# Optimization experiments

Measured on AMD Instinct MI355X. Metric: run time of the kernel, lower is better.

The kernel has to match this reference:

```python
import jax, jax.numpy as jnp
import numpy as np

T, D, I, E, K = 2048, 768, 2048, 8, 2


def setup_inputs() -> dict:
    key = jax.random.key(0)
    ks = jax.random.split(key, 9)
    x = jax.random.normal(ks[0], (T, D), jnp.float32)
    router_weight = jax.random.normal(ks[1], (E, D), jnp.float32) * 0.02
    shared_w_gate = jax.random.normal(ks[2], (I, D), jnp.float32) * 0.02
    shared_w_up = jax.random.normal(ks[3], (I, D), jnp.float32) * 0.02
    shared_w_down = jax.random.normal(ks[4], (D, I), jnp.float32) * 0.02
    # ternary quantized expert weights in {-1, 0, 1}
    expert_q_gate = jax.random.randint(ks[5], (E, I, D), 0, 3, jnp.int32) - 1
    expert_q_up = jax.random.randint(ks[6], (E, I, D), 0, 3, jnp.int32) - 1
    expert_q_down = jax.random.randint(ks[7], (E, D, I), 0, 3, jnp.int32) - 1
    # per-expert, per-matrix dequant scales (gate, up, down)
    expert_scales = jax.random.uniform(ks[8], (E, 3), jnp.float32) * 0.05 + 0.01
    return {
        "x": x,
        "router_weight": router_weight,
        "shared_w_gate": shared_w_gate,
        "shared_w_up": shared_w_up,
        "shared_w_down": shared_w_down,
        "expert_q_gate": expert_q_gate,
        "expert_q_up": expert_q_up,
        "expert_q_down": expert_q_down,
        "expert_scales": expert_scales,
        "top_k": K,
    }


def _swiglu(x, wg, wu, wd):
    # down( silu(gate(x)) * up(x) )
    return (jax.nn.silu(x @ wg.T) * (x @ wu.T)) @ wd.T


def reference(x, router_weight, shared_w_gate, shared_w_up, shared_w_down,
              expert_q_gate, expert_q_up, expert_q_down, expert_scales, top_k):
    # --- router: softmax -> top-k -> renormalize ---
    probs = jax.nn.softmax(x @ router_weight.T, axis=-1)            # [T, E]
    vals, idx = jax.lax.top_k(probs, top_k)                          # [T, K]
    vals = vals / jnp.sum(vals, axis=-1, keepdims=True)
    n_experts = router_weight.shape[0]
    # combine weights as dense [T, E] gate (one-hot scatter of top-k probs)
    gate = jnp.sum(jax.nn.one_hot(idx, n_experts, dtype=x.dtype) * vals[..., None], axis=1)

    # --- dequantize paged ternary experts: w = ternary * scale ---
    wg = expert_q_gate.astype(x.dtype) * expert_scales[:, 0, None, None]  # [E, I, D]
    wu = expert_q_up.astype(x.dtype) * expert_scales[:, 1, None, None]    # [E, I, D]
    wd = expert_q_down.astype(x.dtype) * expert_scales[:, 2, None, None]  # [E, D, I]

    # --- expert SwiGLU, computed per expert and combined with the gate ---
    h = jax.nn.silu(jnp.einsum('td,eid->tei', x, wg)) * jnp.einsum('td,eid->tei', x, wu)
    expert_out = jnp.einsum('tei,edi->ted', h, wd)                   # [T, E, D]
    moe_out = jnp.einsum('te,ted->td', gate, expert_out)             # [T, D]

    # --- always-on shared expert ---
    shared_out = _swiglu(x, shared_w_gate, shared_w_up, shared_w_down)
    return shared_out + moe_out
```

## Files before the change

### kernel.cpp

```cpp
#include <hip/hip_runtime.h>
#include <hip/hip_bf16.h>

#define TDIM 2048
#define DDIM 768
#define IDIM 2048
#define NEXP 8

typedef __bf16 v8bf __attribute__((ext_vector_type(8)));
typedef float v4f __attribute__((ext_vector_type(4)));

#define MFMA_B16(A,B,C) __builtin_amdgcn_mfma_f32_16x16x32_bf16(A,B,C,0,0,0)

typedef __attribute__((address_space(1))) const unsigned int* gas_t;
typedef __attribute__((address_space(3))) unsigned int* las_t;

__device__ __forceinline__ void gload16(const void* g, void* l) {
  __builtin_amdgcn_global_load_lds((gas_t)g, (las_t)l, 16, 0, 0);
}

__global__ __launch_bounds__(64)
void router_kernel(const float* __restrict__ x, const float* __restrict__ rw,
                   int* __restrict__ cnt, int* __restrict__ lists, float* __restrict__ wt)
{
  const int t = blockIdx.x;
  const int lane = threadIdx.x;
  const float* xp = x + (size_t)t * DDIM;
  float4 xv0 = *(const float4*)(xp + lane * 4);
  float4 xv1 = *(const float4*)(xp + 256 + lane * 4);
  float4 xv2 = *(const float4*)(xp + 512 + lane * 4);
  float logit[NEXP];
#pragma unroll
  for (int e = 0; e < NEXP; ++e) {
    const float* w = rw + (size_t)e * DDIM;
    float4 w0 = *(const float4*)(w + lane * 4);
    float4 w1 = *(const float4*)(w + 256 + lane * 4);
    float4 w2 = *(const float4*)(w + 512 + lane * 4);
    float p = xv0.x * w0.x + xv0.y * w0.y + xv0.z * w0.z + xv0.w * w0.w
            + xv1.x * w1.x + xv1.y * w1.y + xv1.z * w1.z + xv1.w * w1.w
            + xv2.x * w2.x + xv2.y * w2.y + xv2.z * w2.z + xv2.w * w2.w;
#pragma unroll
    for (int off = 32; off > 0; off >>= 1) p += __shfl_down(p, off, 64);
    logit[e] = p;
  }
  if (lane == 0) {
    float m = logit[0];
#pragma unroll
    for (int e = 1; e < NEXP; ++e) m = fmaxf(m, logit[e]);
    float pr[NEXP];
#pragma unroll
    for (int e = 0; e < NEXP; ++e) pr[e] = expf(logit[e] - m);
    int i0 = 0; float v0 = pr[0];
#pragma unroll
    for (int e = 1; e < NEXP; ++e) if (pr[e] > v0) { v0 = pr[e]; i0 = e; }
    int i1 = -1; float v1 = -1.f;
#pragma unroll
    for (int e = 0; e < NEXP; ++e) if (e != i0 && pr[e] > v1) { v1 = pr[e]; i1 = e; }
    float inv = 1.f / (v0 + v1);
    int p0 = atomicAdd(&cnt[i0], 1);
    lists[i0 * TDIM + p0] = t * 2;
    wt[t * 2] = v0 * inv;
    int p1 = atomicAdd(&cnt[i1], 1);
    lists[i1 * TDIM + p1] = t * 2 + 1;
    wt[t * 2 + 1] = v1 * inv;
  }
}

template<bool ISINT>
__global__ __launch_bounds__(256)
void pack_tiles_kernel(const void* __restrict__ srcv, __hip_bfloat16* __restrict__ dst,
                       int NT, int KT)
{
  const int b = blockIdx.x;
  const int kt = b % KT;
  const int nt = (b / KT) % NT;
  const int e  = b / (KT * NT);
  const int N  = NT * 128;
  const int Kk = KT * 64;
  const int tid = threadIdx.x;
  __hip_bfloat16* dbase = dst + (size_t)b * 8192;
#pragma unroll
  for (int p = 0; p < 4; ++p) {
    const int q = p * 256 + tid;
    const int row = q >> 3;
    const int cb = ((q & 7) * 16) ^ ((row & 7) << 4);
    const int k = kt * 64 + (cb >> 1);
    const size_t srcoff = ((size_t)e * N + (nt * 128 + row)) * Kk + k;
    v8bf v;
    if constexpr (ISINT) {
      const int* s = (const int*)srcv + srcoff;
      int4 a0 = *(const int4*)s;
      int4 a1 = *(const int4*)(s + 4);
      v[0] = (__bf16)(float)a0.x; v[1] = (__bf16)(float)a0.y;
      v[2] = (__bf16)(float)a0.z; v[3] = (__bf16)(float)a0.w;
      v[4] = (__bf16)(float)a1.x; v[5] = (__bf16)(float)a1.y;
      v[6] = (__bf16)(float)a1.z; v[7] = (__bf16)(float)a1.w;
    } else {
      const float* s = (const float*)srcv + srcoff;
      float4 a0 = *(const float4*)s;
      float4 a1 = *(const float4*)(s + 4);
      v[0] = (__bf16)a0.x; v[1] = (__bf16)a0.y; v[2] = (__bf16)a0.z; v[3] = (__bf16)a0.w;
      v[4] = (__bf16)a1.x; v[5] = (__bf16)a1.y; v[6] = (__bf16)a1.z; v[7] = (__bf16)a1.w;
    }
    *(v8bf*)(dbase + (size_t)q * 8) = v;
  }
}

__global__ __launch_bounds__(256)
void pack_x_kernel(const float* __restrict__ src, __hip_bfloat16* __restrict__ dst)
{
  const size_t i = ((size_t)blockIdx.x * 256 + threadIdx.x) * 8;
  float4 a0 = *(const float4*)(src + i);
  float4 a1 = *(const float4*)(src + i + 4);
  v8bf v;
  v[0] = (__bf16)a0.x; v[1] = (__bf16)a0.y; v[2] = (__bf16)a0.z; v[3] = (__bf16)a0.w;
  v[4] = (__bf16)a1.x; v[5] = (__bf16)a1.y; v[6] = (__bf16)a1.z; v[7] = (__bf16)a1.w;
  *(v8bf*)(dst + i) = v;
}

__global__ __launch_bounds__(256)
void gateup_kernel(const __hip_bfloat16* __restrict__ xb,
                   const __hip_bfloat16* __restrict__ wgT, const __hip_bfloat16* __restrict__ wuT,
                   const __hip_bfloat16* __restrict__ sgT, const __hip_bfloat16* __restrict__ suT,
                   const float* __restrict__ es,
                   const int* __restrict__ cnt, const int* __restrict__ lists,
                   __hip_bfloat16* __restrict__ he, __hip_bfloat16* __restrict__ hs)
{
  const int b = blockIdx.x;
  int tm, tn, count;
  const __hip_bfloat16 *wg, *wu;
  const int* listE = nullptr;
  __hip_bfloat16* hout;
  float sg, su;
  if (b < 2048) {
    const int e = b >> 8; tm = (b >> 4) & 15; tn = b & 15;
    count = cnt[e];
    if (tm * 128 >= count) return;
    wg = wgT + (size_t)(e * 16 + tn) * (12 * 8192);
    wu = wuT + (size_t)(e * 16 + tn) * (12 * 8192);
    listE = lists + e * TDIM;
    sg = es[e * 3 + 0]; su = es[e * 3 + 1];
    hout = he;
  } else {
    const int b2 = b - 2048; tm = b2 >> 4; tn = b2 & 15;
    count = TDIM;
    wg = sgT + (size_t)tn * (12 * 8192);
    wu = suT + (size_t)tn * (12 * 8192);
    sg = 1.f; su = 1.f;
    hout = hs;
  }

  __shared__ __align__(16) char As[16384];
  __shared__ __align__(16) char Bg[16384];
  __shared__ __align__(16) char Bu[16384];

  const int tid = threadIdx.x;
  const int lane = tid & 63;
  const int wid = tid >> 6;
  const int wr = wid >> 1, wc = wid & 1;
  const int lr16 = lane & 15, hk = lane >> 4;
  const int xorm = (lr16 & 7) << 4;

  const int cA = (((lane & 7) ^ (lane >> 3)) << 4);
  const char* aptr[4];
#pragma unroll
  for (int p = 0; p < 4; ++p) {
    const int row = p * 32 + wid * 8 + (lane >> 3);
    const int rg = tm * 128 + row;
    int tok;
    if (listE) { const int idx = rg < count ? rg : count - 1; tok = listE[idx] >> 1; }
    else tok = rg;
    aptr[p] = (const char*)xb + (size_t)tok * (DDIM * 2) + cA;
  }
  const char* bgp = (const char*)wg + wid * 1024 + lane * 16;
  const char* bup = (const char*)wu + wid * 1024 + lane * 16;
  char* ldsA  = As + wid * 1024;
  char* ldsBg = Bg + wid * 1024;
  char* ldsBu = Bu + wid * 1024;

  v4f ag[4][4] = {};
  v4f au[4][4] = {};

  for (int kt = 0; kt < 12; ++kt) {
#pragma unroll
    for (int p = 0; p < 4; ++p) gload16(aptr[p] + kt * 128, ldsA + p * 4096);
#pragma unroll
    for (int p = 0; p < 4; ++p) gload16(bgp + kt * 16384 + p * 4096, ldsBg + p * 4096);
#pragma unroll
    for (int p = 0; p < 4; ++p) gload16(bup + kt * 16384 + p * 4096, ldsBu + p * 4096);
    __syncthreads();
#pragma unroll
    for (int ks = 0; ks < 2; ++ks) {
      const int colb = (ks * 64 + hk * 16) ^ xorm;
      v8bf fa[4];
#pragma unroll
      for (int m = 0; m < 4; ++m)
        fa[m] = *(const v8bf*)(As + (wr * 64 + m * 16 + lr16) * 128 + colb);
#pragma unroll
      for (int n = 0; n < 4; ++n) {
        v8bf fg = *(const v8bf*)(Bg + (wc * 64 + n * 16 + lr16) * 128 + colb);
        v8bf fu = *(const v8bf*)(Bu + (wc * 64 + n * 16 + lr16) * 128 + colb);
#pragma unroll
        for (int m = 0; m < 4; ++m) {
          ag[m][n] = MFMA_B16(fa[m], fg, ag[m][n]);
          au[m][n] = MFMA_B16(fa[m], fu, au[m][n]);
        }
      }
    }
    __syncthreads();
  }

#pragma unroll
  for (int m = 0; m < 4; ++m) {
#pragma unroll
    for (int j = 0; j < 4; ++j) {
      const int rl = wr * 64 + m * 16 + hk * 4 + j;
      const int rg = tm * 128 + rl;
      if (rg >= count) continue;
      const size_t drow = listE ? (size_t)listE[rg] : (size_t)rg;
      __hip_bfloat16* dst = hout + drow * IDIM + tn * 128 + wc * 64 + lr16;
#pragma unroll
      for (int n = 0; n < 4; ++n) {
        const float g = ag[m][n][j] * sg;
        const float u = au[m][n][j] * su;
        const float h = g / (1.f + __expf(-g)) * u;
        dst[n * 16] = __float2bfloat16(h);
      }
    }
  }
}

__global__ __launch_bounds__(256)
void down_kernel(const __hip_bfloat16* __restrict__ he, const __hip_bfloat16* __restrict__ hs,
                 const __hip_bfloat16* __restrict__ wdT, const __hip_bfloat16* __restrict__ sdT,
                 const float* __restrict__ es, const float* __restrict__ wt,
                 const int* __restrict__ cnt, const int* __restrict__ lists,
                 float* __restrict__ out)
{
  const int b = blockIdx.x;
  int tm, tn, count;
  const __hip_bfloat16 *wd, *asrc;
  const int* listE = nullptr;
  float sd;
  if (b < 768) {
    const int e = b / 96; const int r = b % 96; tm = r / 6; tn = r % 6;
    count = cnt[e];
    if (tm * 128 >= count) return;
    wd = wdT + (size_t)(e * 6 + tn) * (32 * 8192);
    listE = lists + e * TDIM;
    sd = es[e * 3 + 2];
    asrc = he;
  } else {
    const int r = b - 768; tm = r / 6; tn = r % 6;
    count = TDIM;
    wd = sdT + (size_t)tn * (32 * 8192);
    sd = 1.f;
    asrc = hs;
  }

  __shared__ __align__(16) char As[16384];
  __shared__ __align__(16) char Bs[16384];

  const int tid = threadIdx.x;
  const int lane = tid & 63;
  const int wid = tid >> 6;
  const int wr = wid >> 1, wc = wid & 1;
  const int lr16 = lane & 15, hk = lane >> 4;
  const int xorm = (lr16 & 7) << 4;

  const int cA = (((lane & 7) ^ (lane >> 3)) << 4);
  const char* aptr[4];
#pragma unroll
  for (int p = 0; p < 4; ++p) {
    const int row = p * 32 + wid * 8 + (lane >> 3);
    const int rg = tm * 128 + row;
    int srow;
    if (listE) { const int idx = rg < count ? rg : count - 1; srow = listE[idx]; }
    else srow = rg;
    aptr[p] = (const char*)asrc + (size_t)srow * (IDIM * 2) + cA;
  }
  const char* bp = (const char*)wd + wid * 1024 + lane * 16;
  char* ldsA = As + wid * 1024;
  char* ldsB = Bs + wid * 1024;

  v4f acc[4][4] = {};

  for (int kt = 0; kt < 32; ++kt) {
#pragma unroll
    for (int p = 0; p < 4; ++p) gload16(aptr[p] + kt * 128, ldsA + p * 4096);
#pragma unroll
    for (int p = 0; p < 4; ++p) gload16(bp + kt * 16384 + p * 4096, ldsB + p * 4096);
    __syncthreads();
#pragma unroll
    for (int ks = 0; ks < 2; ++ks) {
      const int colb = (ks * 64 + hk * 16) ^ xorm;
      v8bf fa[4];
#pragma unroll
      for (int m = 0; m < 4; ++m)
        fa[m] = *(const v8bf*)(As + (wr * 64 + m * 16 + lr16) * 128 + colb);
#pragma unroll
      for (int n = 0; n < 4; ++n) {
        v8bf fb = *(const v8bf*)(Bs + (wc * 64 + n * 16 + lr16) * 128 + colb);
#pragma unroll
        for (int m = 0; m < 4; ++m) acc[m][n] = MFMA_B16(fa[m], fb, acc[m][n]);
      }
    }
    __syncthreads();
  }

#pragma unroll
  for (int m = 0; m < 4; ++m) {
#pragma unroll
    for (int j = 0; j < 4; ++j) {
      const int rl = wr * 64 + m * 16 + hk * 4 + j;
      const int rg = tm * 128 + rl;
      if (rg >= count) continue;
      int tok; float w;
      if (listE) { const int slot = listE[rg]; tok = slot >> 1; w = wt[slot] * sd; }
      else { tok = rg; w = 1.f; }
      float* dst = out + (size_t)tok * DDIM + tn * 128 + wc * 64 + lr16;
#pragma unroll
      for (int n = 0; n < 4; ++n) atomicAdd(dst + n * 16, acc[m][n][j] * w);
    }
  }
}

extern "C" void kernel_launch(void* const* d_in, const int* in_sizes, int n_in,
                              void* d_out, int out_size, void* d_ws, size_t ws_size,
                              hipStream_t stream)
{
  const float* x   = (const float*)d_in[0];
  const float* rw  = (const float*)d_in[1];
  const float* swg = (const float*)d_in[2];
  const float* swu = (const float*)d_in[3];
  const float* swd = (const float*)d_in[4];
  const int*   qg  = (const int*)d_in[5];
  const int*   qu  = (const int*)d_in[6];
  const int*   qd  = (const int*)d_in[7];
  const float* es  = (const float*)d_in[8];
  float* out = (float*)d_out;

  char* ws = (char*)d_ws;
  size_t off = 0;
  auto alloc = [&](size_t bytes) { void* p = ws + off; off = (off + bytes + 255) & ~(size_t)255; return p; };
  int*   cnt   = (int*)alloc(NEXP * 4);
  int*   lists = (int*)alloc((size_t)NEXP * TDIM * 4);
  float* wt    = (float*)alloc((size_t)2 * TDIM * 4);
  __hip_bfloat16* xb  = (__hip_bfloat16*)alloc((size_t)TDIM * DDIM * 2);
  __hip_bfloat16* wgT = (__hip_bfloat16*)alloc((size_t)NEXP * 16 * 12 * 8192 * 2);
  __hip_bfloat16* wuT = (__hip_bfloat16*)alloc((size_t)NEXP * 16 * 12 * 8192 * 2);
  __hip_bfloat16* wdT = (__hip_bfloat16*)alloc((size_t)NEXP * 6 * 32 * 8192 * 2);
  __hip_bfloat16* sgT = (__hip_bfloat16*)alloc((size_t)16 * 12 * 8192 * 2);
  __hip_bfloat16* suT = (__hip_bfloat16*)alloc((size_t)16 * 12 * 8192 * 2);
  __hip_bfloat16* sdT = (__hip_bfloat16*)alloc((size_t)6 * 32 * 8192 * 2);
  __hip_bfloat16* hs  = (__hip_bfloat16*)alloc((size_t)TDIM * IDIM * 2);
  __hip_bfloat16* he  = (__hip_bfloat16*)alloc((size_t)2 * TDIM * IDIM * 2);

  hipMemsetAsync(cnt, 0, NEXP * 4, stream);
  hipMemsetAsync(out, 0, (size_t)TDIM * DDIM * 4, stream);

  router_kernel<<<TDIM, 64, 0, stream>>>(x, rw, cnt, lists, wt);
  pack_x_kernel<<<(TDIM * DDIM) / 2048, 256, 0, stream>>>(x, xb);
  pack_tiles_kernel<true><<<NEXP * 16 * 12, 256, 0, stream>>>(qg, wgT, 16, 12);
  pack_tiles_kernel<true><<<NEXP * 16 * 12, 256, 0, stream>>>(qu, wuT, 16, 12);
  pack_tiles_kernel<true><<<NEXP * 6 * 32, 256, 0, stream>>>(qd, wdT, 6, 32);
  pack_tiles_kernel<false><<<16 * 12, 256, 0, stream>>>(swg, sgT, 16, 12);
  pack_tiles_kernel<false><<<16 * 12, 256, 0, stream>>>(swu, suT, 16, 12);
  pack_tiles_kernel<false><<<6 * 32, 256, 0, stream>>>(swd, sdT, 6, 32);

  gateup_kernel<<<2048 + 256, 256, 0, stream>>>(xb, wgT, wuT, sgT, suT, es, cnt, lists, he, hs);
  down_kernel<<<768 + 96, 256, 0, stream>>>(he, hs, wdT, sdT, es, wt, cnt, lists, out);
}
```

Baseline: 422.9 us.

## Fuse pack kernels into one launch and halve GEMM N-tiles for more blocks

Merges the six weight-packing launches and the x-to-bf16 conversion into a single kernel that dispatches on block index, which removes per-launch overhead and lets the small conversions run alongside each other. The gate/up and down GEMM kernels now use 128x64 output tiles instead of 128x128 by addressing half of each packed 128-row weight tile, doubling the block count. Smaller LDS and accumulator footprints plus occupancy hints in launch_bounds are meant to keep more blocks resident and balance the uneven per-expert work. The cost is that each A tile is loaded from global memory twice as often and there are more atomic-add blocks in the down projection.

```diff
diff --git a/kernel.cpp b/kernel.cpp
--- a/kernel.cpp
+++ b/kernel.cpp
@@ -65,19 +65,41 @@
   }
 }
 
-template<bool ISINT>
 __global__ __launch_bounds__(256)
-void pack_tiles_kernel(const void* __restrict__ srcv, __hip_bfloat16* __restrict__ dst,
-                       int NT, int KT)
+void pack_all_kernel(const int* __restrict__ qg, const int* __restrict__ qu,
+                     const int* __restrict__ qd,
+                     const float* __restrict__ sg, const float* __restrict__ su,
+                     const float* __restrict__ sd, const float* __restrict__ x,
+                     __hip_bfloat16* __restrict__ wgT, __hip_bfloat16* __restrict__ wuT,
+                     __hip_bfloat16* __restrict__ wdT, __hip_bfloat16* __restrict__ sgT,
+                     __hip_bfloat16* __restrict__ suT, __hip_bfloat16* __restrict__ sdT,
+                     __hip_bfloat16* __restrict__ xb)
 {
   const int b = blockIdx.x;
-  const int kt = b % KT;
-  const int nt = (b / KT) % NT;
-  const int e  = b / (KT * NT);
+  const int tid = threadIdx.x;
+  if (b >= 5184) {
+    const size_t i = (size_t)(b - 5184) * 2048 + tid * 8;
+    float4 a0 = *(const float4*)(x + i);
+    float4 a1 = *(const float4*)(x + i + 4);
+    v8bf v;
+    v[0] = (__bf16)a0.x; v[1] = (__bf16)a0.y; v[2] = (__bf16)a0.z; v[3] = (__bf16)a0.w;
+    v[4] = (__bf16)a1.x; v[5] = (__bf16)a1.y; v[6] = (__bf16)a1.z; v[7] = (__bf16)a1.w;
+    *(v8bf*)(xb + i) = v;
+    return;
+  }
+  const void* src; __hip_bfloat16* dst; int NT, KT, isint, tile;
+  if (b < 1536)      { src = qg; dst = wgT; NT = 16; KT = 12; isint = 1; tile = b; }
+  else if (b < 3072) { src = qu; dst = wuT; NT = 16; KT = 12; isint = 1; tile = b - 1536; }
+  else if (b < 4608) { src = qd; dst = wdT; NT = 6;  KT = 32; isint = 1; tile = b - 3072; }
+  else if (b < 4800) { src = sg; dst = sgT; NT = 16; KT = 12; isint = 0; tile = b - 4608; }
+  else if (b < 4992) { src = su; dst = suT; NT = 16; KT = 12; isint = 0; tile = b - 4800; }
+  else               { src = sd; dst = sdT; NT = 6;  KT = 32; isint = 0; tile = b - 4992; }
+  const int kt = tile % KT;
+  const int nt = (tile / KT) % NT;
+  const int e  = tile / (KT * NT);
   const int N  = NT * 128;
   const int Kk = KT * 64;
-  const int tid = threadIdx.x;
-  __hip_bfloat16* dbase = dst + (size_t)b * 8192;
+  __hip_bfloat16* dbase = dst + (size_t)tile * 8192;
 #pragma unroll
   for (int p = 0; p < 4; ++p) {
     const int q = p * 256 + tid;
@@ -86,8 +108,8 @@
     const int k = kt * 64 + (cb >> 1);
     const size_t srcoff = ((size_t)e * N + (nt * 128 + row)) * Kk + k;
     v8bf v;
-    if constexpr (ISINT) {
-      const int* s = (const int*)srcv + srcoff;
+    if (isint) {
+      const int* s = (const int*)src + srcoff;
       int4 a0 = *(const int4*)s;
       int4 a1 = *(const int4*)(s + 4);
       v[0] = (__bf16)(float)a0.x; v[1] = (__bf16)(float)a0.y;
@@ -95,7 +117,7 @@
       v[4] = (__bf16)(float)a1.x; v[5] = (__bf16)(float)a1.y;
       v[6] = (__bf16)(float)a1.z; v[7] = (__bf16)(float)a1.w;
     } else {
-      const float* s = (const float*)srcv + srcoff;
+      const float* s = (const float*)src + srcoff;
       float4 a0 = *(const float4*)s;
       float4 a1 = *(const float4*)(s + 4);
       v[0] = (__bf16)a0.x; v[1] = (__bf16)a0.y; v[2] = (__bf16)a0.z; v[3] = (__bf16)a0.w;
@@ -105,19 +127,7 @@
   }
 }
 
-__global__ __launch_bounds__(256)
-void pack_x_kernel(const float* __restrict__ src, __hip_bfloat16* __restrict__ dst)
-{
-  const size_t i = ((size_t)blockIdx.x * 256 + threadIdx.x) * 8;
-  float4 a0 = *(const float4*)(src + i);
-  float4 a1 = *(const float4*)(src + i + 4);
-  v8bf v;
-  v[0] = (__bf16)a0.x; v[1] = (__bf16)a0.y; v[2] = (__bf16)a0.z; v[3] = (__bf16)a0.w;
-  v[4] = (__bf16)a1.x; v[5] = (__bf16)a1.y; v[6] = (__bf16)a1.z; v[7] = (__bf16)a1.w;
-  *(v8bf*)(dst + i) = v;
-}
-
-__global__ __launch_bounds__(256)
+__global__ __launch_bounds__(256, 3)
 void gateup_kernel(const __hip_bfloat16* __restrict__ xb,
                    const __hip_bfloat16* __restrict__ wgT, const __hip_bfloat16* __restrict__ wuT,
                    const __hip_bfloat16* __restrict__ sgT, const __hip_bfloat16* __restrict__ suT,
@@ -127,38 +137,39 @@
 {
   const int b = blockIdx.x;
   int tm, tn, count;
-  const __hip_bfloat16 *wg, *wu;
+  const char *wg, *wu;
   const int* listE = nullptr;
   __hip_bfloat16* hout;
   float sg, su;
-  if (b < 2048) {
-    const int e = b >> 8; tm = (b >> 4) & 15; tn = b & 15;
+  if (b < 4096) {
+    const int e = b >> 9; tm = (b >> 5) & 15; tn = b & 31;
     count = cnt[e];
     if (tm * 128 >= count) return;
-    wg = wgT + (size_t)(e * 16 + tn) * (12 * 8192);
-    wu = wuT + (size_t)(e * 16 + tn) * (12 * 8192);
+    const size_t base = (size_t)(e * 16 + (tn >> 1)) * (12 * 16384) + (tn & 1) * 8192;
+    wg = (const char*)wgT + base;
+    wu = (const char*)wuT + base;
     listE = lists + e * TDIM;
     sg = es[e * 3 + 0]; su = es[e * 3 + 1];
     hout = he;
   } else {
-    const int b2 = b - 2048; tm = b2 >> 4; tn = b2 & 15;
+    const int b2 = b - 4096; tm = b2 >> 5; tn = b2 & 31;
     count = TDIM;
-    wg = sgT + (size_t)tn * (12 * 8192);
-    wu = suT + (size_t)tn * (12 * 8192);
+    const size_t base = (size_t)(tn >> 1) * (12 * 16384) + (tn & 1) * 8192;
+    wg = (const char*)sgT + base;
+    wu = (const char*)suT + base;
     sg = 1.f; su = 1.f;
     hout = hs;
   }
 
   __shared__ __align__(16) char As[16384];
-  __shared__ __align__(16) char Bg[16384];
-  __shared__ __align__(16) char Bu[16384];
+  __shared__ __align__(16) char Bg[8192];
+  __shared__ __align__(16) char Bu[8192];
 
   const int tid = threadIdx.x;
   const int lane = tid & 63;
   const int wid = tid >> 6;
   const int wr = wid >> 1, wc = wid & 1;
   const int lr16 = lane & 15, hk = lane >> 4;
-  const int xorm = (lr16 & 7) << 4;
 
   const int cA = (((lane & 7) ^ (lane >> 3)) << 4);
   const char* aptr[4];
@@ -171,34 +182,38 @@
     else tok = rg;
     aptr[p] = (const char*)xb + (size_t)tok * (DDIM * 2) + cA;
   }
-  const char* bgp = (const char*)wg + wid * 1024 + lane * 16;
-  const char* bup = (const char*)wu + wid * 1024 + lane * 16;
+  const char* bgp = wg + wid * 1024 + lane * 16;
+  const char* bup = wu + wid * 1024 + lane * 16;
   char* ldsA  = As + wid * 1024;
   char* ldsBg = Bg + wid * 1024;
   char* ldsBu = Bu + wid * 1024;
 
-  v4f ag[4][4] = {};
-  v4f au[4][4] = {};
+  v4f ag[4][2] = {};
+  v4f au[4][2] = {};
 
   for (int kt = 0; kt < 12; ++kt) {
 #pragma unroll
     for (int p = 0; p < 4; ++p) gload16(aptr[p] + kt * 128, ldsA + p * 4096);
 #pragma unroll
-    for (int p = 0; p < 4; ++p) gload16(bgp + kt * 16384 + p * 4096, ldsBg + p * 4096);
-#pragma unroll
-    for (int p = 0; p < 4; ++p) gload16(bup + kt * 16384 + p * 4096, ldsBu + p * 4096);
+    for (int p = 0; p < 2; ++p) gload16(bgp + kt * 16384 + p * 4096, ldsBg + p * 4096);
+#pragma unroll
+    for (int p = 0; p < 2; ++p) gload16(bup + kt * 16384 + p * 4096, ldsBu + p * 4096);
     __syncthreads();
 #pragma unroll
     for (int ks = 0; ks < 2; ++ks) {
-      const int colb = (ks * 64 + hk * 16) ^ xorm;
+      const int colb = ks * 64 + hk * 16;
       v8bf fa[4];
 #pragma unroll
-      for (int m = 0; m < 4; ++m)
-        fa[m] = *(const v8bf*)(As + (wr * 64 + m * 16 + lr16) * 128 + colb);
-#pragma unroll
-      for (int n = 0; n < 4; ++n) {
-        v8bf fg = *(const v8bf*)(Bg + (wc * 64 + n * 16 + lr16) * 128 + colb);
-        v8bf fu = *(const v8bf*)(Bu + (wc * 64 + n * 16 + lr16) * 128 + colb);
+      for (int m = 0; m < 4; ++m) {
+        const int r = wr * 64 + m * 16 + lr16;
+        fa[m] = *(const v8bf*)(As + r * 128 + (colb ^ ((r & 7) << 4)));
+      }
+#pragma unroll
+      for (int n = 0; n < 2; ++n) {
+        const int r = wc * 32 + n * 16 + lr16;
+        const int sb = r * 128 + (colb ^ ((r & 7) << 4));
+        v8bf fg = *(const v8bf*)(Bg + sb);
+        v8bf fu = *(const v8bf*)(Bu + sb);
 #pragma unroll
         for (int m = 0; m < 4; ++m) {
           ag[m][n] = MFMA_B16(fa[m], fg, ag[m][n]);
@@ -217,9 +232,9 @@
       const int rg = tm * 128 + rl;
       if (rg >= count) continue;
       const size_t drow = listE ? (size_t)listE[rg] : (size_t)rg;
-      __hip_bfloat16* dst = hout + drow * IDIM + tn * 128 + wc * 64 + lr16;
-#pragma unroll
-      for (int n = 0; n < 4; ++n) {
+      __hip_bfloat16* dst = hout + drow * IDIM + tn * 64 + wc * 32 + lr16;
+#pragma unroll
+      for (int n = 0; n < 2; ++n) {
         const float g = ag[m][n][j] * sg;
         const float u = au[m][n][j] * su;
         const float h = g / (1.f + __expf(-g)) * u;
@@ -229,7 +244,7 @@
   }
 }
 
-__global__ __launch_bounds__(256)
+__global__ __launch_bounds__(256, 4)
 void down_kernel(const __hip_bfloat16* __restrict__ he, const __hip_bfloat16* __restrict__ hs,
                  const __hip_bfloat16* __restrict__ wdT, const __hip_bfloat16* __restrict__ sdT,
                  const float* __restrict__ es, const float* __restrict__ wt,
@@ -238,34 +253,34 @@
 {
   const int b = blockIdx.x;
   int tm, tn, count;
-  const __hip_bfloat16 *wd, *asrc;
+  const char* wd;
+  const __hip_bfloat16* asrc;
   const int* listE = nullptr;
   float sd;
-  if (b < 768) {
-    const int e = b / 96; const int r = b % 96; tm = r / 6; tn = r % 6;
+  if (b < 1536) {
+    const int e = b / 192; const int r = b % 192; tm = r / 12; tn = r % 12;
     count = cnt[e];
     if (tm * 128 >= count) return;
-    wd = wdT + (size_t)(e * 6 + tn) * (32 * 8192);
+    wd = (const char*)wdT + (size_t)(e * 6 + (tn >> 1)) * (32 * 16384) + (tn & 1) * 8192;
     listE = lists + e * TDIM;
     sd = es[e * 3 + 2];
     asrc = he;
   } else {
-    const int r = b - 768; tm = r / 6; tn = r % 6;
+    const int r = b - 1536; tm = r / 12; tn = r % 12;
     count = TDIM;
-    wd = sdT + (size_t)tn * (32 * 8192);
+    wd = (const char*)sdT + (size_t)(tn >> 1) * (32 * 16384) + (tn & 1) * 8192;
     sd = 1.f;
     asrc = hs;
   }
 
   __shared__ __align__(16) char As[16384];
-  __shared__ __align__(16) char Bs[16384];
+  __shared__ __align__(16) char Bs[8192];
 
   const int tid = threadIdx.x;
   const int lane = tid & 63;
   const int wid = tid >> 6;
   const int wr = wid >> 1, wc = wid & 1;
   const int lr16 = lane & 15, hk = lane >> 4;
-  const int xorm = (lr16 & 7) << 4;
 
   const int cA = (((lane & 7) ^ (lane >> 3)) << 4);
   const char* aptr[4];
@@ -278,28 +293,31 @@
     else srow = rg;
     aptr[p] = (const char*)asrc + (size_t)srow * (IDIM * 2) + cA;
   }
-  const char* bp = (const char*)wd + wid * 1024 + lane * 16;
+  const char* bp = wd + wid * 1024 + lane * 16;
   char* ldsA = As + wid * 1024;
   char* ldsB = Bs + wid * 1024;
 
-  v4f acc[4][4] = {};
+  v4f acc[4][2] = {};
 
   for (int kt = 0; kt < 32; ++kt) {
 #pragma unroll
     for (int p = 0; p < 4; ++p) gload16(aptr[p] + kt * 128, ldsA + p * 4096);
 #pragma unroll
-    for (int p = 0; p < 4; ++p) gload16(bp + kt * 16384 + p * 4096, ldsB + p * 4096);
+    for (int p = 0; p < 2; ++p) gload16(bp + kt * 16384 + p * 4096, ldsB + p * 4096);
     __syncthreads();
 #pragma unroll
     for (int ks = 0; ks < 2; ++ks) {
-      const int colb = (ks * 64 + hk * 16) ^ xorm;
+      const int colb = ks * 64 + hk * 16;
       v8bf fa[4];
 #pragma unroll
-      for (int m = 0; m < 4; ++m)
-        fa[m] = *(const v8bf*)(As + (wr * 64 + m * 16 + lr16) * 128 + colb);
-#pragma unroll
-      for (int n = 0; n < 4; ++n) {
-        v8bf fb = *(const v8bf*)(Bs + (wc * 64 + n * 16 + lr16) * 128 + colb);
+      for (int m = 0; m < 4; ++m) {
+        const int r = wr * 64 + m * 16 + lr16;
+        fa[m] = *(const v8bf*)(As + r * 128 + (colb ^ ((r & 7) << 4)));
+      }
+#pragma unroll
+      for (int n = 0; n < 2; ++n) {
+        const int r = wc * 32 + n * 16 + lr16;
+        v8bf fb = *(const v8bf*)(Bs + r * 128 + (colb ^ ((r & 7) << 4)));
 #pragma unroll
         for (int m = 0; m < 4; ++m) acc[m][n] = MFMA_B16(fa[m], fb, acc[m][n]);
       }
@@ -317,9 +335,9 @@
       int tok; float w;
       if (listE) { const int slot = listE[rg]; tok = slot >> 1; w = wt[slot] * sd; }
       else { tok = rg; w = 1.f; }
-      float* dst = out + (size_t)tok * DDIM + tn * 128 + wc * 64 + lr16;
-#pragma unroll
-      for (int n = 0; n < 4; ++n) atomicAdd(dst + n * 16, acc[m][n][j] * w);
+      float* dst = out + (size_t)tok * DDIM + tn * 64 + wc * 32 + lr16;
+#pragma unroll
+      for (int n = 0; n < 2; ++n) atomicAdd(dst + n * 16, acc[m][n][j] * w);
     }
   }
 }
@@ -359,14 +377,9 @@
   hipMemsetAsync(out, 0, (size_t)TDIM * DDIM * 4, stream);
 
   router_kernel<<<TDIM, 64, 0, stream>>>(x, rw, cnt, lists, wt);
-  pack_x_kernel<<<(TDIM * DDIM) / 2048, 256, 0, stream>>>(x, xb);
-  pack_tiles_kernel<true><<<NEXP * 16 * 12, 256, 0, stream>>>(qg, wgT, 16, 12);
-  pack_tiles_kernel<true><<<NEXP * 16 * 12, 256, 0, stream>>>(qu, wuT, 16, 12);
-  pack_tiles_kernel<true><<<NEXP * 6 * 32, 256, 0, stream>>>(qd, wdT, 6, 32);
-  pack_tiles_kernel<false><<<16 * 12, 256, 0, stream>>>(swg, sgT, 16, 12);
-  pack_tiles_kernel<false><<<16 * 12, 256, 0, stream>>>(swu, suT, 16, 12);
-  pack_tiles_kernel<false><<<6 * 32, 256, 0, stream>>>(swd, sdT, 6, 32);
-
-  gateup_kernel<<<2048 + 256, 256, 0, stream>>>(xb, wgT, wuT, sgT, suT, es, cnt, lists, he, hs);
-  down_kernel<<<768 + 96, 256, 0, stream>>>(he, hs, wdT, sdT, es, wt, cnt, lists, out);
-}
+  pack_all_kernel<<<5184 + 768, 256, 0, stream>>>(qg, qu, qd, swg, swu, swd, x,
+                                                  wgT, wuT, wdT, sgT, suT, sdT, xb);
+
+  gateup_kernel<<<4096 + 512, 256, 0, stream>>>(xb, wgT, wuT, sgT, suT, es, cnt, lists, he, hs);
+  down_kernel<<<1536 + 192, 256, 0, stream>>>(he, hs, wdT, sdT, es, wt, cnt, lists, out);
+}
```

Result: faster. 369.4 us (-12.7%).
